# Optimization experiments

Measured on AMD Instinct MI355X. Metric: run time of the kernel, lower is better.

The kernel has to match this reference:

```python
import jax, jax.numpy as jnp
import numpy as np

EPS = 1e-7  # entropy eps
DIAG_EPS = 1e-8
LEAK = 0.2  # LeakyReLU slope


def _entropy(p):
    # EntropyLoss: mean over leading dims of -sum(p*log(p+eps), -1)
    return jnp.mean(-jnp.sum(p * jnp.log(p + EPS), axis=-1))


def setup_inputs() -> dict:
    key = jax.random.key(0)
    ks = jax.random.split(key, 7)
    B, S, C, F, E, H = 256, 6, 80, 2048, 300, 1024
    x = jax.random.normal(ks[0], (B, F, 14, 14), dtype=jnp.float32)
    inp = jax.random.normal(ks[1], (C, E), dtype=jnp.float32) * 0.1
    y = (jax.random.uniform(ks[2], (B, C)) < 0.1).astype(jnp.float32)
    # persistent co-occurrence buffer (non-negative counts)
    comatrix = jax.random.uniform(ks[3], (S, C, C), dtype=jnp.float32) * 50.0
    W_scene = jax.random.normal(ks[4], (F, S), dtype=jnp.float32) * 0.02
    W1 = jax.random.uniform(ks[5], (E, H), dtype=jnp.float32, minval=-1, maxval=1) / np.sqrt(H)
    W2 = jax.random.uniform(ks[6], (H, F), dtype=jnp.float32, minval=-1, maxval=1) / np.sqrt(F)
    return {"x": x, "inp": inp, "y": y, "comatrix": comatrix,
            "W_scene": W_scene, "W1": W1, "W2": W2}


def reference(x, inp, y, comatrix, W_scene, W1, W2):
    B = x.shape[0]
    S, C, _ = comatrix.shape
    # backbone output -> MaxPool2d(14,14) == global max over the 14x14 map
    img_feats = jnp.max(x, axis=(2, 3))                       # [B, F]
    scene_scores = img_feats @ W_scene                        # [B, S]
    scene_probs = jax.nn.softmax(scene_scores, axis=-1)
    # --- training-path comatrix scatter update (comat_smooth=False) ---
    batch_comats = y[:, :, None] * y[:, None, :]              # [B, C, C]
    ids = jnp.argmax(scene_probs, axis=-1)                    # [B]
    comatrix = comatrix + jnp.zeros_like(comatrix).at[ids].add(batch_comats)
    # --- entropy terms ---
    sample_en = _entropy(scene_probs)
    max_en = _entropy(jnp.full((S,), 1.0 / S, dtype=scene_probs.dtype))
    batch_en = (max_en - _entropy(jnp.mean(scene_probs, axis=0))) * 100.0
    # --- comatrix2prob: row-normalize by diagonal, force diag=1 ---
    diag = jnp.diagonal(comatrix, axis1=1, axis2=2)[:, :, None]  # [S, C, 1]
    comat = comatrix / (diag + DIAG_EPS)
    eye = jnp.eye(C, dtype=comat.dtype)
    comat = comat * (1.0 - eye) + eye
    comats = comat[ids]                                       # gather [B, C, C]
    # --- gen_adj: adj = D^{-1/2} A^T D^{-1/2}, D = rowsums(A) ---
    D = jax.lax.rsqrt(jnp.sum(comats, axis=2))                # [B, C]
    adjs = D[:, :, None] * jnp.swapaxes(comats, 1, 2) * D[:, None, :]
    # --- 2-layer GCN ---
    h = adjs @ (inp @ W1)                                     # [B, C, 1024]
    h = jnp.where(h > 0, h, LEAK * h)
    h = adjs @ (h @ W2)                                       # [B, C, 2048]
    output = jnp.einsum('bcf,bf->bc', h, img_feats)           # [B, C]
    return (output, scene_probs, sample_en, batch_en, comats)
```

## Files before the change

kernel.cpp:

```cpp
#include <hip/hip_runtime.h>
#include <math.h>

#define B_ 256
#define S_ 6
#define C_ 80
#define F_ 2048
#define E_ 300
#define H_ 1024
#define EPS_ 1e-7f
#define DEPS_ 1e-8f
#define LEAK_ 0.2f

#define IMG_OFF   0u
#define Z_OFF     524288u
#define COMAT_OFF 606208u
#define ADJA_OFF  644608u
#define G_OFF     683008u
#define PART_OFF  1174528u
#define IDS_OFF   5368832u
#define MP_OFF    5369088u
#define SEN_OFF   5369094u

#define OUT0_OFF 0
#define PROB_OFF 20480
#define SEN_OUT  22016
#define BEN_OUT  22017
#define CMTS_OFF 22018

__global__ __launch_bounds__(256) void k_maxpool(const float* __restrict__ x,
                                                 float* __restrict__ img) {
    int pair = blockIdx.x * 4 + (threadIdx.x >> 6);
    int lane = threadIdx.x & 63;
    const float4* xp = (const float4*)x + (size_t)pair * 49;
    float m = -INFINITY;
    if (lane < 49) {
        float4 v = xp[lane];
        m = fmaxf(fmaxf(v.x, v.y), fmaxf(v.z, v.w));
    }
#pragma unroll
    for (int off = 32; off >= 1; off >>= 1) m = fmaxf(m, __shfl_xor(m, off));
    if (lane == 0) img[pair] = m;
}

__global__ __launch_bounds__(256) void k_scene(const float* __restrict__ img,
                                               const float* __restrict__ Ws,
                                               float* __restrict__ probs_out,
                                               int* __restrict__ ids,
                                               float* __restrict__ mp,
                                               float* __restrict__ sen) {
    __shared__ float red[6][256];
    int b = blockIdx.x, tid = threadIdx.x;
    float acc[6] = {0, 0, 0, 0, 0, 0};
#pragma unroll
    for (int i = 0; i < 8; i++) {
        int f = tid + i * 256;
        float a = img[b * F_ + f];
#pragma unroll
        for (int s = 0; s < 6; s++) acc[s] += a * Ws[f * 6 + s];
    }
    for (int s = 0; s < 6; s++) red[s][tid] = acc[s];
    __syncthreads();
    for (int off = 128; off > 0; off >>= 1) {
        if (tid < off)
            for (int s = 0; s < 6; s++) red[s][tid] += red[s][tid + off];
        __syncthreads();
    }
    if (tid == 0) {
        float sc[6], mx = -INFINITY;
        for (int s = 0; s < 6; s++) { sc[s] = red[s][0]; mx = fmaxf(mx, sc[s]); }
        float sum = 0.f;
        for (int s = 0; s < 6; s++) { sc[s] = expf(sc[s] - mx); sum += sc[s]; }
        float inv = 1.0f / sum;
        float p[6], ent = 0.f;
        int best = 0; float bv = -1.f;
        for (int s = 0; s < 6; s++) {
            p[s] = sc[s] * inv;
            probs_out[b * 6 + s] = p[s];
            ent -= p[s] * logf(p[s] + EPS_);
            if (p[s] > bv) { bv = p[s]; best = s; }
            atomicAdd(&mp[s], p[s]);
        }
        atomicAdd(sen, ent);
        ids[b] = best;
    }
}

__global__ __launch_bounds__(256) void k_comat(const float* __restrict__ y,
                                               const float* __restrict__ cm_in,
                                               const int* __restrict__ ids,
                                               float* __restrict__ comat,
                                               float* __restrict__ adjA) {
    int s = blockIdx.x, tid = threadIdx.x;
    __shared__ unsigned long long colq[80][4];
    __shared__ float cm[6400];
    __shared__ float diag[80], Dn[80];
    __shared__ int idsL[256];
    idsL[tid] = ids[tid];
    __syncthreads();
    int wave = tid >> 6, lane = tid & 63;
    int b = tid;
    bool ok = (idsL[b] == s);
    for (int i = 0; i < 80; i++) {
        bool pred = ok && (y[b * 80 + i] != 0.0f);
        unsigned long long mk = __ballot(pred);
        if (lane == 0) colq[i][wave] = mk;
    }
    __syncthreads();
    for (int p = tid; p < 6400; p += 256) {
        int i = p / 80, j = p - i * 80;
        int cnt = 0;
#pragma unroll
        for (int w = 0; w < 4; w++) cnt += __popcll(colq[i][w] & colq[j][w]);
        cm[p] = cm_in[s * 6400 + p] + (float)cnt;
    }
    __syncthreads();
    if (tid < 80) diag[tid] = cm[tid * 81];
    __syncthreads();
    for (int p = tid; p < 6400; p += 256) {
        int i = p / 80, j = p - i * 80;
        float v = (i == j) ? 1.0f : cm[p] / (diag[i] + DEPS_);
        cm[p] = v;
        comat[s * 6400 + p] = v;
    }
    __syncthreads();
    if (tid < 80) {
        float rs = 0.f;
        for (int j = 0; j < 80; j++) rs += cm[tid * 80 + j];
        Dn[tid] = 1.0f / sqrtf(rs);
    }
    __syncthreads();
    for (int p = tid; p < 6400; p += 256) {
        int i = p / 80, j = p - i * 80;
        adjA[s * 6400 + p] = Dn[i] * cm[j * 80 + i] * Dn[j];
    }
}

__global__ __launch_bounds__(256) void k_z(const float* __restrict__ inp,
                                           const float* __restrict__ W1,
                                           float* __restrict__ Z) {
    int c = blockIdx.x >> 2;
    int h = ((blockIdx.x & 3) << 8) + threadIdx.x;
    float acc = 0.f;
    for (int e = 0; e < E_; e++) acc += inp[c * E_ + e] * W1[e * H_ + h];
    Z[c * H_ + h] = acc;
}

__global__ __launch_bounds__(256) void k_g(const float* __restrict__ adjA,
                                           const float* __restrict__ Z,
                                           float* __restrict__ g) {
    int s = blockIdx.x / 80, c = blockIdx.x % 80;
    const float* row = adjA + (s * 80 + c) * 80;
    const float4* Z4 = (const float4*)Z;
    float4 acc = {0, 0, 0, 0};
    for (int j = 0; j < 80; j++) {
        float a = row[j];
        float4 z = Z4[j * 256 + threadIdx.x];
        acc.x += a * z.x; acc.y += a * z.y; acc.z += a * z.z; acc.w += a * z.w;
    }
    acc.x = acc.x > 0.f ? acc.x : LEAK_ * acc.x;
    acc.y = acc.y > 0.f ? acc.y : LEAK_ * acc.y;
    acc.z = acc.z > 0.f ? acc.z : LEAK_ * acc.z;
    acc.w = acc.w > 0.f ? acc.w : LEAK_ * acc.w;
    ((float4*)g)[(s * 80 + c) * 256 + threadIdx.x] = acc;
}

__global__ __launch_bounds__(256) void k_ugemm(const float* __restrict__ A,
                                               const float* __restrict__ Bm,
                                               float* __restrict__ part) {
    __shared__ float As[16 * 132];
    __shared__ float Bs[16 * 132];
    int tid = threadIdx.x;
    int m0 = blockIdx.y * 128, h0 = blockIdx.x * 128;
    int kbase = blockIdx.z * 128;
    float acc[8][8];
#pragma unroll
    for (int i = 0; i < 8; i++)
#pragma unroll
        for (int j = 0; j < 8; j++) acc[i][j] = 0.f;
    int r0 = (tid >> 4) << 3, c0 = (tid & 15) << 3;
    for (int st = 0; st < 8; st++) {
        int kc = kbase + st * 16;
#pragma unroll
        for (int l = 0; l < 2; l++) {
            int fid = tid + (l << 8);
            int r = fid >> 2, kq = fid & 3;
            float4 av = *(const float4*)(A + (size_t)(m0 + r) * 2048 + kc + (kq << 2));
            float4 bv = *(const float4*)(Bm + (size_t)(h0 + r) * 2048 + kc + (kq << 2));
            int kk = kq << 2;
            As[(kk + 0) * 132 + r] = av.x; As[(kk + 1) * 132 + r] = av.y;
            As[(kk + 2) * 132 + r] = av.z; As[(kk + 3) * 132 + r] = av.w;
            Bs[(kk + 0) * 132 + r] = bv.x; Bs[(kk + 1) * 132 + r] = bv.y;
            Bs[(kk + 2) * 132 + r] = bv.z; Bs[(kk + 3) * 132 + r] = bv.w;
        }
        __syncthreads();
#pragma unroll
        for (int k = 0; k < 16; k++) {
            float4 a0 = *(const float4*)&As[k * 132 + r0];
            float4 a1 = *(const float4*)&As[k * 132 + r0 + 4];
            float4 b0 = *(const float4*)&Bs[k * 132 + c0];
            float4 b1 = *(const float4*)&Bs[k * 132 + c0 + 4];
            float ar[8] = {a0.x, a0.y, a0.z, a0.w, a1.x, a1.y, a1.z, a1.w};
            float br[8] = {b0.x, b0.y, b0.z, b0.w, b1.x, b1.y, b1.z, b1.w};
#pragma unroll
            for (int i = 0; i < 8; i++)
#pragma unroll
                for (int j = 0; j < 8; j++) acc[i][j] += ar[i] * br[j];
        }
        __syncthreads();
    }
    float* pu = part + (size_t)blockIdx.z * 262144;
#pragma unroll
    for (int i = 0; i < 8; i++) {
        int row = m0 + r0 + i;
        float4 v0 = {acc[i][0], acc[i][1], acc[i][2], acc[i][3]};
        float4 v1 = {acc[i][4], acc[i][5], acc[i][6], acc[i][7]};
        *(float4*)(pu + (size_t)row * 1024 + h0 + c0) = v0;
        *(float4*)(pu + (size_t)row * 1024 + h0 + c0 + 4) = v1;
    }
}

__global__ __launch_bounds__(320) void k_out(const float* __restrict__ part,
                                             const float* __restrict__ g,
                                             const float* __restrict__ adjA,
                                             const int* __restrict__ ids,
                                             float* __restrict__ out0) {
    __shared__ float ul[1024];
    __shared__ float tp[320];
    __shared__ float tv[80];
    int b = blockIdx.x, tid = threadIdx.x;
    int s = ids[b];
    for (int h = tid; h < 1024; h += 320) {
        float a = 0.f;
#pragma unroll
        for (int z = 0; z < 16; z++) a += part[z * 262144 + b * 1024 + h];
        ul[h] = a;
    }
    __syncthreads();
    int c = tid >> 2, q = tid & 3;
    const float4* gp = (const float4*)(g + (s * 80 + c) * 1024 + q * 256);
    const float4* up = (const float4*)(ul + q * 256);
    float a = 0.f;
    for (int k = 0; k < 64; k++) {
        float4 gv = gp[k];
        float4 uv = up[k];
        a += gv.x * uv.x + gv.y * uv.y + gv.z * uv.z + gv.w * uv.w;
    }
    tp[tid] = a;
    __syncthreads();
    if (tid < 80) tv[tid] = tp[tid * 4] + tp[tid * 4 + 1] + tp[tid * 4 + 2] + tp[tid * 4 + 3];
    __syncthreads();
    if (tid < 80) {
        const float* ar = adjA + (s * 80 + tid) * 80;
        float o = 0.f;
        for (int j = 0; j < 80; j++) o += ar[j] * tv[j];
        out0[b * 80 + tid] = o;
    }
}

__global__ __launch_bounds__(256) void k_gather(const float* __restrict__ comat,
                                                const int* __restrict__ ids,
                                                float* __restrict__ cmts) {
    int b = blockIdx.x;
    int s = ids[b];
    const float2* src = (const float2*)(comat + s * 6400);
    float2* dst = (float2*)(cmts + (size_t)b * 6400);
    for (int i = threadIdx.x; i < 3200; i += 256) dst[i] = src[i];
}

__global__ void k_final(const float* __restrict__ mp, const float* __restrict__ sen,
                        float* __restrict__ o_sen, float* __restrict__ o_ben) {
    if (threadIdx.x == 0 && blockIdx.x == 0) {
        *o_sen = *sen / 256.0f;
        float ent = 0.f;
        for (int s = 0; s < 6; s++) {
            float q = mp[s] / 256.0f;
            ent -= q * logf(q + EPS_);
        }
        float invS = 1.0f / 6.0f;
        float men = -6.0f * (invS * logf(invS + EPS_));
        *o_ben = (men - ent) * 100.0f;
    }
}

extern "C" void kernel_launch(void* const* d_in, const int* in_sizes, int n_in,
                              void* d_out, int out_size, void* d_ws, size_t ws_size,
                              hipStream_t stream) {
    const float* x    = (const float*)d_in[0];
    const float* inp  = (const float*)d_in[1];
    const float* y    = (const float*)d_in[2];
    const float* cmin = (const float*)d_in[3];
    const float* Ws   = (const float*)d_in[4];
    const float* W1   = (const float*)d_in[5];
    const float* W2   = (const float*)d_in[6];
    float* out = (float*)d_out;
    float* W = (float*)d_ws;

    float* img   = W + IMG_OFF;
    float* Z     = W + Z_OFF;
    float* comat = W + COMAT_OFF;
    float* adjA  = W + ADJA_OFF;
    float* g     = W + G_OFF;
    float* part  = W + PART_OFF;
    int*   ids   = (int*)(W + IDS_OFF);
    float* mp    = W + MP_OFF;
    float* sen   = W + SEN_OFF;

    hipMemsetAsync(mp, 0, 7 * sizeof(float), stream);
    k_maxpool<<<131072, 256, 0, stream>>>(x, img);
    k_scene<<<256, 256, 0, stream>>>(img, Ws, out + PROB_OFF, ids, mp, sen);
    k_comat<<<6, 256, 0, stream>>>(y, cmin, ids, comat, adjA);
    k_z<<<320, 256, 0, stream>>>(inp, W1, Z);
    k_g<<<480, 256, 0, stream>>>(adjA, Z, g);
    k_ugemm<<<dim3(8, 2, 16), 256, 0, stream>>>(img, W2, part);
    k_out<<<256, 320, 0, stream>>>(part, g, adjA, ids, out + OUT0_OFF);
    k_gather<<<256, 256, 0, stream>>>(comat, ids, out + CMTS_OFF);
    k_final<<<1, 64, 0, stream>>>(mp, sen, out + SEN_OUT, out + BEN_OUT);
}
```

Measured before the change: 674.3 us.

## Precompute adj·g per scene and halve ugemm row tile for more blocks

Adds a k_g2 kernel that multiplies the per-scene adjacency by g once for all six scenes, so k_out becomes a single dot product per class against the precomputed rows instead of a dot product followed by an 80x80 adjacency matvec per batch element. k_out now uses wave-level shuffle reductions with 256 threads. k_ugemm switches to 64-row tiles, doubling the grid to 512 blocks for better occupancy. This adds an extra launch and a small extra buffer of G2, but removes per-batch adjacency work and reduces per-thread accumulator registers.

```diff
diff --git a/kernel.cpp b/kernel.cpp
--- a/kernel.cpp
+++ b/kernel.cpp
@@ -16,10 +16,11 @@
 #define COMAT_OFF 606208u
 #define ADJA_OFF  644608u
 #define G_OFF     683008u
-#define PART_OFF  1174528u
-#define IDS_OFF   5368832u
-#define MP_OFF    5369088u
-#define SEN_OFF   5369094u
+#define G2_OFF    1174528u
+#define PART_OFF  1666048u
+#define IDS_OFF   5860352u
+#define MP_OFF    5860608u
+#define SEN_OFF   5860614u
 
 #define OUT0_OFF 0
 #define PROB_OFF 20480
@@ -164,45 +165,63 @@
     ((float4*)g)[(s * 80 + c) * 256 + threadIdx.x] = acc;
 }
 
+__global__ __launch_bounds__(256) void k_g2(const float* __restrict__ adjA,
+                                            const float* __restrict__ g,
+                                            float* __restrict__ G2) {
+    int s = blockIdx.x / 80, c = blockIdx.x % 80;
+    const float* row = adjA + (s * 80 + c) * 80;
+    const float4* g4 = (const float4*)(g + (size_t)s * 80 * 1024);
+    float4 acc = {0, 0, 0, 0};
+    for (int j = 0; j < 80; j++) {
+        float a = row[j];
+        float4 z = g4[j * 256 + threadIdx.x];
+        acc.x += a * z.x; acc.y += a * z.y; acc.z += a * z.z; acc.w += a * z.w;
+    }
+    ((float4*)G2)[(s * 80 + c) * 256 + threadIdx.x] = acc;
+}
+
 __global__ __launch_bounds__(256) void k_ugemm(const float* __restrict__ A,
                                                const float* __restrict__ Bm,
                                                float* __restrict__ part) {
-    __shared__ float As[16 * 132];
+    __shared__ float As[16 * 68];
     __shared__ float Bs[16 * 132];
     int tid = threadIdx.x;
-    int m0 = blockIdx.y * 128, h0 = blockIdx.x * 128;
+    int m0 = blockIdx.y * 64, h0 = blockIdx.x * 128;
     int kbase = blockIdx.z * 128;
-    float acc[8][8];
-#pragma unroll
-    for (int i = 0; i < 8; i++)
+    float acc[4][8];
+#pragma unroll
+    for (int i = 0; i < 4; i++)
 #pragma unroll
         for (int j = 0; j < 8; j++) acc[i][j] = 0.f;
-    int r0 = (tid >> 4) << 3, c0 = (tid & 15) << 3;
+    int r0 = (tid >> 4) << 2, c0 = (tid & 15) << 3;
     for (int st = 0; st < 8; st++) {
         int kc = kbase + st * 16;
+        {
+            int r = tid >> 2, kq = tid & 3;
+            float4 av = *(const float4*)(A + (size_t)(m0 + r) * 2048 + kc + (kq << 2));
+            int kk = kq << 2;
+            As[(kk + 0) * 68 + r] = av.x; As[(kk + 1) * 68 + r] = av.y;
+            As[(kk + 2) * 68 + r] = av.z; As[(kk + 3) * 68 + r] = av.w;
+        }
 #pragma unroll
         for (int l = 0; l < 2; l++) {
             int fid = tid + (l << 8);
             int r = fid >> 2, kq = fid & 3;
-            float4 av = *(const float4*)(A + (size_t)(m0 + r) * 2048 + kc + (kq << 2));
             float4 bv = *(const float4*)(Bm + (size_t)(h0 + r) * 2048 + kc + (kq << 2));
             int kk = kq << 2;
-            As[(kk + 0) * 132 + r] = av.x; As[(kk + 1) * 132 + r] = av.y;
-            As[(kk + 2) * 132 + r] = av.z; As[(kk + 3) * 132 + r] = av.w;
             Bs[(kk + 0) * 132 + r] = bv.x; Bs[(kk + 1) * 132 + r] = bv.y;
             Bs[(kk + 2) * 132 + r] = bv.z; Bs[(kk + 3) * 132 + r] = bv.w;
         }
         __syncthreads();
 #pragma unroll
         for (int k = 0; k < 16; k++) {
-            float4 a0 = *(const float4*)&As[k * 132 + r0];
-            float4 a1 = *(const float4*)&As[k * 132 + r0 + 4];
+            float4 a0 = *(const float4*)&As[k * 68 + r0];
             float4 b0 = *(const float4*)&Bs[k * 132 + c0];
             float4 b1 = *(const float4*)&Bs[k * 132 + c0 + 4];
-            float ar[8] = {a0.x, a0.y, a0.z, a0.w, a1.x, a1.y, a1.z, a1.w};
+            float ar[4] = {a0.x, a0.y, a0.z, a0.w};
             float br[8] = {b0.x, b0.y, b0.z, b0.w, b1.x, b1.y, b1.z, b1.w};
 #pragma unroll
-            for (int i = 0; i < 8; i++)
+            for (int i = 0; i < 4; i++)
 #pragma unroll
                 for (int j = 0; j < 8; j++) acc[i][j] += ar[i] * br[j];
         }
@@ -210,7 +229,7 @@
     }
     float* pu = part + (size_t)blockIdx.z * 262144;
 #pragma unroll
-    for (int i = 0; i < 8; i++) {
+    for (int i = 0; i < 4; i++) {
         int row = m0 + r0 + i;
         float4 v0 = {acc[i][0], acc[i][1], acc[i][2], acc[i][3]};
         float4 v1 = {acc[i][4], acc[i][5], acc[i][6], acc[i][7]};
@@ -219,41 +238,34 @@
     }
 }
 
-__global__ __launch_bounds__(320) void k_out(const float* __restrict__ part,
-                                             const float* __restrict__ g,
-                                             const float* __restrict__ adjA,
+__global__ __launch_bounds__(256) void k_out(const float* __restrict__ part,
+                                             const float* __restrict__ G2,
                                              const int* __restrict__ ids,
                                              float* __restrict__ out0) {
     __shared__ float ul[1024];
-    __shared__ float tp[320];
-    __shared__ float tv[80];
     int b = blockIdx.x, tid = threadIdx.x;
     int s = ids[b];
-    for (int h = tid; h < 1024; h += 320) {
+    for (int h = tid; h < 1024; h += 256) {
         float a = 0.f;
 #pragma unroll
         for (int z = 0; z < 16; z++) a += part[z * 262144 + b * 1024 + h];
         ul[h] = a;
     }
     __syncthreads();
-    int c = tid >> 2, q = tid & 3;
-    const float4* gp = (const float4*)(g + (s * 80 + c) * 1024 + q * 256);
-    const float4* up = (const float4*)(ul + q * 256);
-    float a = 0.f;
-    for (int k = 0; k < 64; k++) {
-        float4 gv = gp[k];
-        float4 uv = up[k];
-        a += gv.x * uv.x + gv.y * uv.y + gv.z * uv.z + gv.w * uv.w;
-    }
-    tp[tid] = a;
-    __syncthreads();
-    if (tid < 80) tv[tid] = tp[tid * 4] + tp[tid * 4 + 1] + tp[tid * 4 + 2] + tp[tid * 4 + 3];
-    __syncthreads();
-    if (tid < 80) {
-        const float* ar = adjA + (s * 80 + tid) * 80;
-        float o = 0.f;
-        for (int j = 0; j < 80; j++) o += ar[j] * tv[j];
-        out0[b * 80 + tid] = o;
+    int wave = tid >> 6, lane = tid & 63;
+    const float4* u4 = (const float4*)ul;
+    for (int c = wave; c < 80; c += 4) {
+        const float4* row = (const float4*)(G2 + (size_t)(s * 80 + c) * 1024);
+        float a = 0.f;
+#pragma unroll
+        for (int t = 0; t < 4; t++) {
+            float4 gv = row[lane + t * 64];
+            float4 uv = u4[lane + t * 64];
+            a += gv.x * uv.x + gv.y * uv.y + gv.z * uv.z + gv.w * uv.w;
+        }
+#pragma unroll
+        for (int off = 32; off >= 1; off >>= 1) a += __shfl_xor(a, off);
+        if (lane == 0) out0[b * 80 + c] = a;
     }
 }
 
@@ -300,6 +312,7 @@
     float* comat = W + COMAT_OFF;
     float* adjA  = W + ADJA_OFF;
     float* g     = W + G_OFF;
+    float* G2    = W + G2_OFF;
     float* part  = W + PART_OFF;
     int*   ids   = (int*)(W + IDS_OFF);
     float* mp    = W + MP_OFF;
@@ -311,8 +324,9 @@
     k_comat<<<6, 256, 0, stream>>>(y, cmin, ids, comat, adjA);
     k_z<<<320, 256, 0, stream>>>(inp, W1, Z);
     k_g<<<480, 256, 0, stream>>>(adjA, Z, g);
-    k_ugemm<<<dim3(8, 2, 16), 256, 0, stream>>>(img, W2, part);
-    k_out<<<256, 320, 0, stream>>>(part, g, adjA, ids, out + OUT0_OFF);
+    k_g2<<<480, 256, 0, stream>>>(adjA, g, G2);
+    k_ugemm<<<dim3(8, 4, 16), 256, 0, stream>>>(img, W2, part);
+    k_out<<<256, 256, 0, stream>>>(part, G2, ids, out + OUT0_OFF);
     k_gather<<<256, 256, 0, stream>>>(comat, ids, out + CMTS_OFF);
     k_final<<<1, 64, 0, stream>>>(mp, sen, out + SEN_OUT, out + BEN_OUT);
 }
```

Result: no change. 678.2 us (+0.6%).
